# Optimization experiments

Hardware: AMD Instinct MI355X
Metric: run time of the kernel (lower is better)

## Reference

```python
import jax, jax.numpy as jnp
import numpy as np

R = 8
TOP_K_A = 2
TOP_K_B = 2
SCALING = 16.0 / R  # lora_alpha / r


def setup_inputs() -> dict:
    key = jax.random.key(0)
    k1, k2, k3, k4, k5 = jax.random.split(key, 5)
    B, S, D_IN, D_OUT, EA, EB = 4, 2048, 4096, 4096, 8, 8
    x = jax.random.normal(k1, (B, S, D_IN), dtype=jnp.float32)
    router_logits_a = jax.random.normal(k2, (B * S, EA), dtype=jnp.float32)
    router_logits_b = jax.random.normal(k3, (B * S, EB), dtype=jnp.float32)
    # nn.Linear(in, r).weight -> [r, in]; stacked per expert: [E_a, r, in]
    Wa = jax.random.normal(k4, (EA, R, D_IN), dtype=jnp.float32) * (1.0 / np.sqrt(D_IN))
    # nn.Linear(r, out).weight -> [out, r]; stacked: [E_b, out, r]
    Wb = jax.random.normal(k5, (EB, D_OUT, R), dtype=jnp.float32) * (1.0 / np.sqrt(R))
    return {"x": x, "router_logits_a": router_logits_a,
            "router_logits_b": router_logits_b, "Wa": Wa, "Wb": Wb}


def reference(x, router_logits_a, router_logits_b, Wa, Wb):
    B, S, D_IN = x.shape
    flat_x = x.reshape(-1, D_IN)  # [T, D_in]

    # --- A experts: dense compute over all experts, then top-k gather ---
    topk_logits_a, topk_idx_a = jax.lax.top_k(router_logits_a, TOP_K_A)
    weights_a = jax.nn.softmax(topk_logits_a, axis=-1)  # [T, k_a]
    a_all = jnp.einsum('ti,eri->ter', flat_x, Wa)  # [T, E_a, r]
    sel_a = jnp.take_along_axis(a_all, topk_idx_a[:, :, None], axis=1)  # [T, k_a, r]
    mid = jnp.sum(sel_a * weights_a[:, :, None], axis=1)  # [T, r]

    # --- B experts: dense compute over all experts, then top-k gather ---
    b_all = jnp.einsum('tr,eor->teo', mid, Wb)  # [T, E_b, D_out]
    topk_logits_b, topk_idx_b = jax.lax.top_k(router_logits_b, TOP_K_B)
    weights_b = jax.nn.softmax(topk_logits_b, axis=-1)  # [T, k_b]
    sel_b = jnp.take_along_axis(b_all, topk_idx_b[:, :, None], axis=1)  # [T, k_b, D_out]
    out_flat = jnp.sum(sel_b * weights_b[:, :, None], axis=1) * SCALING  # [T, D_out]
    output = out_flat.reshape(B, S, -1)

    # --- load-balancing aux losses (torch.var is unbiased) ---
    probs_a = jnp.mean(jax.nn.softmax(router_logits_a, axis=-1), axis=0)
    probs_b = jnp.mean(jax.nn.softmax(router_logits_b, axis=-1), axis=0)
    aux_loss_a = Wa.shape[0] * jnp.var(probs_a, ddof=1)
    aux_loss_b = Wb.shape[0] * jnp.var(probs_b, ddof=1)
    return output, aux_loss_a, aux_loss_b
```

## Files before the change

kernel.cpp:

```cpp
#include <hip/hip_runtime.h>

#define T_TOK 8192
#define D_IN  4096
#define D_OUT 4096

typedef _Float16 h2 __attribute__((ext_vector_type(2)));
typedef _Float16 h4 __attribute__((ext_vector_type(4)));
typedef _Float16 h8 __attribute__((ext_vector_type(8)));
typedef float    f4v __attribute__((ext_vector_type(4)));

__device__ __forceinline__ h2 pkrtz(float a, float b) {
    auto r = __builtin_amdgcn_cvt_pkrtz(a, b);
    h2 o; __builtin_memcpy(&o, &r, 4); return o;
}
__device__ __forceinline__ h8 cvt8(float4 f0, float4 f1) {
    h2 p0 = pkrtz(f0.x, f0.y), p1 = pkrtz(f0.z, f0.w);
    h2 p2 = pkrtz(f1.x, f1.y), p3 = pkrtz(f1.z, f1.w);
    return (h8){p0.x, p0.y, p1.x, p1.y, p2.x, p2.y, p3.x, p3.y};
}

__device__ __forceinline__ void gl_lds16(const void* g, void* l) {
    __builtin_amdgcn_global_load_lds(
        (const __attribute__((address_space(1))) unsigned int*)g,
        (__attribute__((address_space(3))) unsigned int*)l, 16, 0, 0);
}


__global__ __launch_bounds__(256)
void prep(const float* __restrict__ Wa, const float* __restrict__ Wb,
          const float* __restrict__ la, const float* __restrict__ lb,
          _Float16* __restrict__ WaB, _Float16* __restrict__ WbB,
          double* __restrict__ pax) {
    const int bid = blockIdx.x, tx = threadIdx.x;
    __shared__ double red[4][16];
    if (bid < 256) {
        int gid = bid * 256 + tx;
        int er = gid >> 10, k0 = (gid & 1023) * 4;
        float4 v = ((const float4*)Wa)[gid];
        h2 p0 = pkrtz(v.x, v.y), p1 = pkrtz(v.z, v.w);
        h4 o = { p0.x, p0.y, p1.x, p1.y };
        int it = k0 >> 7, ks = (k0 >> 5) & 3, kf = (k0 >> 3) & 3;
        int g = er >> 4, mr = er & 15;
        *(h4*)(WaB + it * 8192 + (ks * 4 + g) * 512 + (kf * 16 + mr) * 8
               + (k0 & 7)) = o;
    } else if (bid < 384) {
        int gid = (bid - 256) * 256 + tx;
        int e = gid >> 12, o = gid & 4095;
        const float4* p = (const float4*)(Wb + ((size_t)e * 4096 + o) * 8);
        h8 v = cvt8(p[0], p[1]);
        int ch = o >> 7, wv = (o >> 4) & 7, mr = o & 15;
        *(h8*)(WbB + (size_t)ch * 8192 + ((e >> 2) * 8 + wv) * 512
               + ((e & 3) * 16 + mr) * 8) = v;
    } else {
        const int ab = bid - 384;
        const int t = ab * 256 + tx;
        double loc[16];
        {
            float l[8];
#pragma unroll
            for (int i = 0; i < 8; ++i) l[i] = la[(size_t)t * 8 + i];
            float m = l[0];
#pragma unroll
            for (int i = 1; i < 8; ++i) m = fmaxf(m, l[i]);
            float s = 0.f, e[8];
#pragma unroll
            for (int i = 0; i < 8; ++i) { e[i] = __expf(l[i] - m); s += e[i]; }
#pragma unroll
            for (int i = 0; i < 8; ++i) loc[i] = (double)(e[i] / s);
        }
        {
            float l[8];
#pragma unroll
            for (int i = 0; i < 8; ++i) l[i] = lb[(size_t)t * 8 + i];
            float m = l[0];
#pragma unroll
            for (int i = 1; i < 8; ++i) m = fmaxf(m, l[i]);
            float s = 0.f, e[8];
#pragma unroll
            for (int i = 0; i < 8; ++i) { e[i] = __expf(l[i] - m); s += e[i]; }
#pragma unroll
            for (int i = 0; i < 8; ++i) loc[8 + i] = (double)(e[i] / s);
        }
        const int lane = tx & 63, wid = tx >> 6;
#pragma unroll
        for (int v = 0; v < 16; ++v) {
            double s = loc[v];
#pragma unroll
            for (int off = 32; off > 0; off >>= 1) s += __shfl_down(s, off, 64);
            if (lane == 0) red[wid][v] = s;
        }
        __syncthreads();
        if (tx < 16)
            pax[ab * 16 + tx] = red[0][tx] + red[1][tx] + red[2][tx] + red[3][tx];
    }
}

__global__ __launch_bounds__(512, 4)
void fused(const float* __restrict__ x, const _Float16* __restrict__ WaB,
           const _Float16* __restrict__ WbB, const float* __restrict__ la,
           const float* __restrict__ lb, float* __restrict__ out,
           const double* __restrict__ pax) {
    __shared__ char S[49152];
    __shared__ float sW0[16], sW1[16], sCb[16][8];
    __shared__ int   sE0[16], sE1[16];
    __shared__ double sl[16];

    const int tx = threadIdx.x, l = tx & 63, w = tx >> 6;
    const int mr = l & 15, kf = l >> 4;
    const int m0 = blockIdx.x * 16;
    const int g  = w & 3;
    const int kh = w >> 2;
    const int er1 = g * 16 + mr;
    float* pLp = (float*)(S + 32768);
    _Float16* MbLp = (_Float16*)(S + 41216);

    f4v acc = (f4v){0.f, 0.f, 0.f, 0.f};

#define STAGE1(IT, BUF) do {                                                   \
    _Pragma("unroll") for (int i_ = 0; i_ < 3; ++i_) {                         \
        int p_ = w * 3 + i_;                                                   \
        if (p_ < 8) {                                                          \
            const char* src_ = (const char*)x + (size_t)(m0 + mr) * 16384      \
                + (size_t)(IT) * 512 + (p_ >> 1) * 128 + kf * 32 + (p_ & 1) * 16; \
            gl_lds16(src_, S + (BUF) * 8192 + p_ * 1024);                      \
        } else {                                                               \
            int q_ = p_ - 8;                                                   \
            const char* src_ = (const char*)WaB + (size_t)(IT) * 16384         \
                + q_ * 1024 + l * 16;                                          \
            gl_lds16(src_, S + 16384 + (BUF) * 16384 + q_ * 1024);             \
        }                                                                      \
    }                                                                          \
  } while (0)

#define CMP1(BUF) do {                                                         \
    _Pragma("unroll") for (int i_ = 0; i_ < 2; ++i_) {                         \
        int ks_ = kh * 2 + i_;                                                 \
        float4 f0_ = *(const float4*)(S + (BUF) * 8192 + (ks_ * 2) * 1024 + l * 16);     \
        float4 f1_ = *(const float4*)(S + (BUF) * 8192 + (ks_ * 2 + 1) * 1024 + l * 16); \
        h8 a_ = cvt8(f0_, f1_);                                                \
        h8 b_ = *(const h8*)(S + 16384 + (BUF) * 16384                         \
                             + (ks_ * 4 + g) * 1024 + l * 16);                 \
        acc = __builtin_amdgcn_mfma_f32_16x16x32_f16(a_, b_, acc, 0, 0, 0);    \
    }                                                                          \
  } while (0)

    STAGE1(0, 0);
    __syncthreads();
#pragma unroll 1
    for (int it = 0; it < 32; ++it) {
        if (it < 31) STAGE1(it + 1, (it & 1) ^ 1);
        CMP1(it & 1);
        __syncthreads();
    }
#undef STAGE1
#undef CMP1

#pragma unroll
    for (int r = 0; r < 4; ++r) pLp[kh * 1056 + (kf * 4 + r) * 66 + er1] = acc[r];
    __syncthreads();

    if (tx < 16) {
        const int t = tx;
        float lg[8];
#pragma unroll
        for (int i = 0; i < 8; ++i) lg[i] = la[(size_t)(m0 + t) * 8 + i];
        int e0 = 0; float b0 = lg[0];
#pragma unroll
        for (int i = 1; i < 8; ++i) if (lg[i] > b0) { b0 = lg[i]; e0 = i; }
        int e1 = -1; float b1 = -1e30f;
#pragma unroll
        for (int i = 0; i < 8; ++i) if (i != e0 && lg[i] > b1) { b1 = lg[i]; e1 = i; }
        float w1 = __expf(b1 - b0), s = 1.f + w1;
        sW0[t] = 1.f / s; sW1[t] = w1 / s; sE0[t] = e0; sE1[t] = e1;

#pragma unroll
        for (int i = 0; i < 8; ++i) lg[i] = lb[(size_t)(m0 + t) * 8 + i];
        int f0 = 0; float c0 = lg[0];
#pragma unroll
        for (int i = 1; i < 8; ++i) if (lg[i] > c0) { c0 = lg[i]; f0 = i; }
        int f1 = -1; float c1 = -1e30f;
#pragma unroll
        for (int i = 0; i < 8; ++i) if (i != f0 && lg[i] > c1) { c1 = lg[i]; f1 = i; }
        float wb1 = __expf(c1 - c0), sb = 1.f + wb1;
        float wb0s = 2.f / sb, wb1s = 2.f * wb1 / sb;
#pragma unroll
        for (int e = 0; e < 8; ++e)
            sCb[t][e] = (e == f0) ? wb0s : (e == f1) ? wb1s : 0.f;
    }
    __syncthreads();

    if (tx < 256) {
        const int t = tx >> 4, gg = tx & 15;
        const float w0 = sW0[t], w1 = sW1[t];
        const int e0 = sE0[t], e1 = sE1[t];
        const float cb = sCb[t][gg >> 1];
        h4 o;
#pragma unroll
        for (int j = 0; j < 4; ++j) {
            int r = (gg * 4 + j) & 7;
            float mid = w0 * (pLp[t * 66 + e0 * 8 + r] + pLp[1056 + t * 66 + e0 * 8 + r])
                      + w1 * (pLp[t * 66 + e1 * 8 + r] + pLp[1056 + t * 66 + e1 * 8 + r]);
            o[j] = (_Float16)(cb * mid);
        }
        *(h4*)(MbLp + ((gg >> 1) * 16 + t) * 8 + (gg & 1) * 4) = o;
    }
    __syncthreads();

    h8 a30 = *(const h8*)(MbLp + ((0 * 4 + kf) * 16 + mr) * 8);
    h8 a31 = *(const h8*)(MbLp + ((1 * 4 + kf) * 16 + mr) * 8);
    float* outp = out + (size_t)(m0 + kf * 4) * D_OUT;

#define STAGE3(CH, BUF) do {                                                   \
    _Pragma("unroll") for (int i_ = 0; i_ < 2; ++i_) {                         \
        int p_ = w * 2 + i_;                                                   \
        const char* src_ = (const char*)WbB + (size_t)(CH) * 16384             \
            + p_ * 1024 + l * 16;                                              \
        gl_lds16(src_, S + (BUF) * 16384 + p_ * 1024);                         \
    }                                                                          \
  } while (0)

#define CMP3(BUF, CH) do {                                                     \
    f4v o0 = (f4v){0.f,0.f,0.f,0.f};                                           \
    h8 b0_ = *(const h8*)(S + (BUF) * 16384 + (0 * 8 + w) * 1024 + l * 16);    \
    h8 b1_ = *(const h8*)(S + (BUF) * 16384 + (1 * 8 + w) * 1024 + l * 16);    \
    o0 = __builtin_amdgcn_mfma_f32_16x16x32_f16(a30, b0_, o0, 0, 0, 0);        \
    o0 = __builtin_amdgcn_mfma_f32_16x16x32_f16(a31, b1_, o0, 0, 0, 0);        \
    int n0_ = (CH) * 128 + w * 16 + mr;                                        \
    _Pragma("unroll") for (int r_ = 0; r_ < 4; ++r_)                           \
        outp[(size_t)r_ * D_OUT + n0_] = o0[r_];                               \
  } while (0)

    STAGE3(0, 0);
    __syncthreads();
#pragma unroll 1
    for (int c = 0; c < 32; ++c) {
        if (c < 31) STAGE3(c + 1, (c & 1) ^ 1);
        CMP3(c & 1, c);
        __syncthreads();
    }
#undef STAGE3
#undef CMP3

    if (blockIdx.x == 0) {
        if (tx < 16) {
            double s = 0.0;
#pragma unroll
            for (int b = 0; b < 32; ++b) s += pax[b * 16 + tx];
            sl[tx] = s;
        }
        __syncthreads();
        if (tx == 0) {
            double pa[8], pb[8], ma = 0.0, mb = 0.0;
            for (int e = 0; e < 8; ++e) { pa[e] = sl[e] / 8192.0;     ma += pa[e] / 8.0; }
            for (int e = 0; e < 8; ++e) { pb[e] = sl[8 + e] / 8192.0; mb += pb[e] / 8.0; }
            double va = 0.0, vb = 0.0;
            for (int e = 0; e < 8; ++e) { double d = pa[e] - ma; va += d * d; }
            for (int e = 0; e < 8; ++e) { double d = pb[e] - mb; vb += d * d; }
            out[(size_t)T_TOK * D_OUT + 0] = (float)(8.0 * va / 7.0);
            out[(size_t)T_TOK * D_OUT + 1] = (float)(8.0 * vb / 7.0);
        }
    }
}

extern "C" void kernel_launch(void* const* d_in, const int* in_sizes, int n_in,
                              void* d_out, int out_size, void* d_ws, size_t ws_size,
                              hipStream_t stream) {
    const float* x  = (const float*)d_in[0];
    const float* la = (const float*)d_in[1];
    const float* lb = (const float*)d_in[2];
    const float* Wa = (const float*)d_in[3];
    const float* Wb = (const float*)d_in[4];
    float* out = (float*)d_out;

    char* ws = (char*)d_ws;
    _Float16* WaB = (_Float16*)ws;
    _Float16* WbB = (_Float16*)(ws + 524288);
    double*   pax = (double*)(ws + 1048576);

    prep<<<416, 256, 0, stream>>>(Wa, Wb, la, lb, WaB, WbB, pax);
    fused<<<512, 512, 0, stream>>>(x, WaB, WbB, la, lb, out, pax);
}
```

Before: 278.2 us.

## Triple-buffer stage-1 loads and stream Wb from registers in stage 3

```diff
diff --git a/kernel.cpp b/kernel.cpp
--- a/kernel.cpp
+++ b/kernel.cpp
@@ -18,6 +18,7 @@
     h2 p2 = pkrtz(f1.x, f1.y), p3 = pkrtz(f1.z, f1.w);
     return (h8){p0.x, p0.y, p1.x, p1.y, p2.x, p2.y, p3.x, p3.y};
 }
+__device__ __forceinline__ h8 as_h8(uint4 u) { h8 b; __builtin_memcpy(&b, &u, 16); return b; }
 
 __device__ __forceinline__ void gl_lds16(const void* g, void* l) {
     __builtin_amdgcn_global_load_lds(
@@ -100,7 +101,7 @@
            const _Float16* __restrict__ WbB, const float* __restrict__ la,
            const float* __restrict__ lb, float* __restrict__ out,
            const double* __restrict__ pax) {
-    __shared__ char S[49152];
+    __shared__ char S[73728];
     __shared__ float sW0[16], sW1[16], sCb[16][8];
     __shared__ int   sE0[16], sE1[16];
     __shared__ double sl[16];
@@ -111,8 +112,8 @@
     const int g  = w & 3;
     const int kh = w >> 2;
     const int er1 = g * 16 + mr;
-    float* pLp = (float*)(S + 32768);
-    _Float16* MbLp = (_Float16*)(S + 41216);
+    float* pLp = (float*)S;
+    _Float16* MbLp = (_Float16*)(S + 8448);
 
     f4v acc = (f4v){0.f, 0.f, 0.f, 0.f};
 
@@ -122,12 +123,12 @@
         if (p_ < 8) {                                                          \
             const char* src_ = (const char*)x + (size_t)(m0 + mr) * 16384      \
                 + (size_t)(IT) * 512 + (p_ >> 1) * 128 + kf * 32 + (p_ & 1) * 16; \
-            gl_lds16(src_, S + (BUF) * 8192 + p_ * 1024);                      \
+            gl_lds16(src_, S + (BUF) * 24576 + p_ * 1024);                     \
         } else {                                                               \
             int q_ = p_ - 8;                                                   \
             const char* src_ = (const char*)WaB + (size_t)(IT) * 16384         \
                 + q_ * 1024 + l * 16;                                          \
-            gl_lds16(src_, S + 16384 + (BUF) * 16384 + q_ * 1024);             \
+            gl_lds16(src_, S + (BUF) * 24576 + 8192 + q_ * 1024);              \
         }                                                                      \
     }                                                                          \
   } while (0)
@@ -135,22 +136,32 @@
 #define CMP1(BUF) do {                                                         \
     _Pragma("unroll") for (int i_ = 0; i_ < 2; ++i_) {                         \
         int ks_ = kh * 2 + i_;                                                 \
-        float4 f0_ = *(const float4*)(S + (BUF) * 8192 + (ks_ * 2) * 1024 + l * 16);     \
-        float4 f1_ = *(const float4*)(S + (BUF) * 8192 + (ks_ * 2 + 1) * 1024 + l * 16); \
+        float4 f0_ = *(const float4*)(S + (BUF) * 24576 + (ks_ * 2) * 1024 + l * 16);     \
+        float4 f1_ = *(const float4*)(S + (BUF) * 24576 + (ks_ * 2 + 1) * 1024 + l * 16); \
         h8 a_ = cvt8(f0_, f1_);                                                \
-        h8 b_ = *(const h8*)(S + 16384 + (BUF) * 16384                         \
+        h8 b_ = *(const h8*)(S + (BUF) * 24576 + 8192                          \
                              + (ks_ * 4 + g) * 1024 + l * 16);                 \
         acc = __builtin_amdgcn_mfma_f32_16x16x32_f16(a_, b_, acc, 0, 0, 0);    \
     }                                                                          \
   } while (0)
 
     STAGE1(0, 0);
-    __syncthreads();
+    STAGE1(1, 1);
+    {
+        int bc = 0;
+        int bs = 2;
 #pragma unroll 1
-    for (int it = 0; it < 32; ++it) {
-        if (it < 31) STAGE1(it + 1, (it & 1) ^ 1);
-        CMP1(it & 1);
-        __syncthreads();
+        for (int it = 0; it < 31; ++it) {
+            asm volatile("s_waitcnt vmcnt(3)" ::: "memory");
+            __builtin_amdgcn_s_barrier();
+            if (it < 30) STAGE1(it + 2, bs);
+            CMP1(bc);
+            bc = (bc == 2) ? 0 : bc + 1;
+            bs = (bs == 2) ? 0 : bs + 1;
+        }
+        asm volatile("s_waitcnt vmcnt(0)" ::: "memory");
+        __builtin_amdgcn_s_barrier();
+        CMP1(1);
     }
 #undef STAGE1
 #undef CMP1
@@ -208,37 +219,32 @@
 
     h8 a30 = *(const h8*)(MbLp + ((0 * 4 + kf) * 16 + mr) * 8);
     h8 a31 = *(const h8*)(MbLp + ((1 * 4 + kf) * 16 + mr) * 8);
+    const uint4* wb4 = (const uint4*)WbB;
     float* outp = out + (size_t)(m0 + kf * 4) * D_OUT;
 
-#define STAGE3(CH, BUF) do {                                                   \
-    _Pragma("unroll") for (int i_ = 0; i_ < 2; ++i_) {                         \
-        int p_ = w * 2 + i_;                                                   \
-        const char* src_ = (const char*)WbB + (size_t)(CH) * 16384             \
-            + p_ * 1024 + l * 16;                                              \
-        gl_lds16(src_, S + (BUF) * 16384 + p_ * 1024);                         \
-    }                                                                          \
-  } while (0)
-
-#define CMP3(BUF, CH) do {                                                     \
+    uint4 C0[2], C1[2];
+#define LDB3(Cd, CH) do {                                                      \
+    Cd[0] = wb4[(size_t)(CH) * 1024 + w * 64 + l];                             \
+    Cd[1] = wb4[(size_t)(CH) * 1024 + 512 + w * 64 + l];                       \
+  } while (0)
+
+#define CMP3(Cs, CH) do {                                                      \
     f4v o0 = (f4v){0.f,0.f,0.f,0.f};                                           \
-    h8 b0_ = *(const h8*)(S + (BUF) * 16384 + (0 * 8 + w) * 1024 + l * 16);    \
-    h8 b1_ = *(const h8*)(S + (BUF) * 16384 + (1 * 8 + w) * 1024 + l * 16);    \
-    o0 = __builtin_amdgcn_mfma_f32_16x16x32_f16(a30, b0_, o0, 0, 0, 0);        \
-    o0 = __builtin_amdgcn_mfma_f32_16x16x32_f16(a31, b1_, o0, 0, 0, 0);        \
+    o0 = __builtin_amdgcn_mfma_f32_16x16x32_f16(a30, as_h8(Cs[0]), o0, 0,0,0); \
+    o0 = __builtin_amdgcn_mfma_f32_16x16x32_f16(a31, as_h8(Cs[1]), o0, 0,0,0); \
     int n0_ = (CH) * 128 + w * 16 + mr;                                        \
     _Pragma("unroll") for (int r_ = 0; r_ < 4; ++r_)                           \
         outp[(size_t)r_ * D_OUT + n0_] = o0[r_];                               \
   } while (0)
 
-    STAGE3(0, 0);
-    __syncthreads();
+    LDB3(C0, 0);
 #pragma unroll 1
-    for (int c = 0; c < 32; ++c) {
-        if (c < 31) STAGE3(c + 1, (c & 1) ^ 1);
-        CMP3(c & 1, c);
-        __syncthreads();
-    }
-#undef STAGE3
+    for (int c = 0; c < 30; c += 2) {
+        LDB3(C1, c + 1); CMP3(C0, c);
+        LDB3(C0, c + 2); CMP3(C1, c + 1);
+    }
+    LDB3(C1, 31); CMP3(C0, 30); CMP3(C1, 31);
+#undef LDB3
 #undef CMP3
 
     if (blockIdx.x == 0) {
```

After: 271.0 us. 2.6% less time.
